# Kernel optimization log

Measured on AMD Instinct MI355X. Metric: run time of the kernel, lower is better.

Reference implementation:

```python
import jax, jax.numpy as jnp
import numpy as np

B, T, C, K = 16, 4096, 64, 1024  # K = codebook rows including pad row 0


def setup_inputs() -> dict:
    key = jax.random.key(0)
    k1, k2, k3 = jax.random.split(key, 3)
    z = jax.random.normal(k1, (B, T, C), dtype=jnp.float32)
    codebook_weight = jax.random.normal(k2, (K, C), dtype=jnp.float32)
    # contiguous valid prefixes of random length (torch loop breaks at first 0)
    lengths = jax.random.randint(k3, (B,), T // 2, T + 1)
    mask = (jnp.arange(T)[None, :] < lengths[:, None]).astype(jnp.float32)[:, :, None]
    return {"z": z, "codebook_weight": codebook_weight, "mask": mask}


def _forward(z, codebook_weight, mask):
    # F.normalize(z, p=2, dim=-1) with eps clamp
    z = z / jnp.clip(jnp.linalg.norm(z, axis=-1, keepdims=True), 1e-12)
    e = jax.lax.stop_gradient(codebook_weight)[1:]  # (K-1, C), detached like torch
    zf = z.reshape(-1, C)                            # (B*T, C)
    # squared euclidean distances: ||z||^2 + ||e||^2 - 2 z e^T
    d = (zf * zf).sum(1, keepdims=True) + (e * e).sum(1)[None, :] - 2.0 * (zf @ e.T)
    idx = jnp.argmin(d, axis=1).reshape(B, T)        # (B, T) codes in [0, K-2]
    # scatter(one-hot) @ e  ==  gather rows of e
    z_q = e[idx] * mask                              # (B, T, C)

    valid_count = mask.sum()
    commitment_loss = (jnp.square(z - jax.lax.stop_gradient(z_q)) * mask).sum() / valid_count

    # straight-through estimator
    z_q = z + z_q - jax.lax.stop_gradient(z)

    m1 = mask[:, 1:, :]
    smoothness_loss = (jnp.square(z_q[:, :-1, :] - z_q[:, 1:, :]) * m1).sum() / m1.sum()

    # --- parallel RLE (replaces the host-side python loop) ---
    # torch loop breaks at first mask==0 -> only contiguous valid prefix matters
    mvalid = jnp.cumprod(mask[..., 0], axis=1) > 0   # (B, T) bool
    change = idx[:, 1:] != idx[:, :-1]
    # position 0 always starts a segment; new segment where code changes inside valid prefix
    is_start = jnp.concatenate(
        [jnp.ones((B, 1), dtype=bool), change & mvalid[:, 1:]], axis=1)  # (B, T)
    # stable argsort puts start positions first, in increasing time order
    order = jnp.argsort(jnp.where(is_start, 0, 1), axis=1)               # (B, T)
    n = is_start.sum(axis=1)                                             # segments per batch
    sel_mask = jnp.arange(T)[None, :] < n[:, None]                        # (B, T)
    sel_pos = jnp.where(sel_mask, order, 0)                               # padded to T
    n_mask = sel_mask.astype(jnp.float32)[..., None]                      # (B, T, 1)
    n_z_q = jnp.take_along_axis(z_q, sel_pos[:, :, None], axis=1) * n_mask
    selected_encodings = jnp.where(
        sel_mask, jnp.take_along_axis(idx, sel_pos, axis=1) + 1, 0)       # (B, T) int
    return smoothness_loss, commitment_loss, z_q, n_z_q, n_mask, selected_encodings


def reference(z, codebook_weight, mask):
    return _forward(z, codebook_weight, mask)
```

## Files before the change

### kernel.cpp

```cpp
#include <hip/hip_runtime.h>
#include <math.h>

typedef __attribute__((ext_vector_type(8))) short short8;
typedef __attribute__((ext_vector_type(4))) float f32x4;

#define B_  16
#define T_  4096
#define C_  64
#define KE_ 1023
#define BT_ (B_ * T_)
#define WINHALF 5e-4f


__device__ __forceinline__ unsigned short f2bf(float x) {
    unsigned int u = __float_as_uint(x);
    unsigned int r = (u + 0x7FFFu + ((u >> 16) & 1u)) >> 16;
    return (unsigned short)r;
}
__device__ __forceinline__ float bf2f(unsigned short h) {
    return __uint_as_float(((unsigned int)h) << 16);
}

typedef __attribute__((address_space(1))) const unsigned int g_u32;
typedef __attribute__((address_space(3))) unsigned int l_u32;
__device__ __forceinline__ void gload16(const void* g, void* l) {
    __builtin_amdgcn_global_load_lds((g_u32*)g, (l_u32*)l, 16, 0, 0);
}

__global__ __launch_bounds__(256) void k_prep(const float* __restrict__ cb,
                                              float* __restrict__ ee,
                                              float* __restrict__ ee2,
                                              unsigned short* __restrict__ Eh,
                                              unsigned short* __restrict__ El,
                                              int* __restrict__ flagcnt) {
    const int k = blockIdx.x * 256 + threadIdx.x;
    if (k == 0) *flagcnt = 0;
    unsigned int* EhU = (unsigned int*)Eh;
    unsigned int* ElU = (unsigned int*)El;
    if (k < KE_) {
        const float* r = cb + (size_t)(k + 1) * C_;
        float s = 0.f;
        #pragma unroll
        for (int c = 0; c < C_; c += 2) {
            const float x0 = r[c], x1 = r[c + 1];
            s = fmaf(x0, x0, s);
            s = fmaf(x1, x1, s);
            const float n0 = -x0, n1 = -x1;
            const unsigned short h0 = f2bf(n0), h1 = f2bf(n1);
            const unsigned short l0 = f2bf(n0 - bf2f(h0));
            const unsigned short l1 = f2bf(n1 - bf2f(h1));
            EhU[k * 32 + c / 2] = (unsigned int)h0 | ((unsigned int)h1 << 16);
            ElU[k * 32 + c / 2] = (unsigned int)l0 | ((unsigned int)l1 << 16);
        }
        ee[k]  = s;
        ee2[k] = 0.5f + 0.5f * s;
    } else {
        #pragma unroll
        for (int c = 0; c < 32; ++c) { EhU[k * 32 + c] = 0u; ElU[k * 32 + c] = 0u; }
        ee[k]  = INFINITY;
        ee2[k] = INFINITY;
    }
}

__global__ __launch_bounds__(256, 2) void k_assign(
    const float* __restrict__ z, const unsigned short* __restrict__ Eh,
    const unsigned short* __restrict__ El, const float* __restrict__ ee2,
    int* __restrict__ kbest, int* __restrict__ flaglist,
    int* __restrict__ flagcnt) {

    __shared__ __align__(16) unsigned short s_eh[2][128 * 64];
    __shared__ __align__(16) unsigned short s_el[2][128 * 64];
    __shared__ float s_ee[2][128];

    const int tid  = threadIdx.x;
    const int wave = tid >> 6;
    const int lane = tid & 63;
    const int col  = lane & 15;
    const int quad = lane >> 4;
    const int Q0   = blockIdx.x * 128 + wave * 32;

    short8 ah[2][2], al[2][2];
    #pragma unroll
    for (int g = 0; g < 2; ++g) {
        const float4* zp = (const float4*)(z + (size_t)(Q0 + g * 16 + col) * C_);
        const float4 f0 = zp[quad * 2];
        const float4 f1 = zp[quad * 2 + 1];
        const float4 f2 = zp[8 + quad * 2];
        const float4 f3 = zp[8 + quad * 2 + 1];
        float xs[16] = {f0.x, f0.y, f0.z, f0.w, f1.x, f1.y, f1.z, f1.w,
                        f2.x, f2.y, f2.z, f2.w, f3.x, f3.y, f3.z, f3.w};
        float ss = 0.f;
        #pragma unroll
        for (int i = 0; i < 16; ++i) ss = fmaf(xs[i], xs[i], ss);
        ss += __shfl_xor(ss, 16);
        ss += __shfl_xor(ss, 32);
        const float inv = 1.f / fmaxf(sqrtf(ss), 1e-12f);
        short8 h0, h1, l0, l1;
        #pragma unroll
        for (int i = 0; i < 8; ++i) {
            const float x = xs[i] * inv;
            const unsigned short hx = f2bf(x);
            h0[i] = (short)hx;
            l0[i] = (short)f2bf(x - bf2f(hx));
            const float y = xs[8 + i] * inv;
            const unsigned short hy = f2bf(y);
            h1[i] = (short)hy;
            l1[i] = (short)f2bf(y - bf2f(hy));
        }
        ah[g][0] = h0; ah[g][1] = h1;
        al[g][0] = l0; al[g][1] = l1;
    }

    float bestv[2][4], secv[2][4];
    int   bkk[2][4];
    #pragma unroll
    for (int g = 0; g < 2; ++g)
        #pragma unroll
        for (int r = 0; r < 4; ++r) {
            bestv[g][r] = INFINITY; secv[g][r] = INFINITY; bkk[g][r] = 0;
        }

    const int srow = tid >> 3;
    const int schk = (tid & 7) ^ (srow & 7);
    const int ldsb = (wave * 8) * 64;

#define STAGE(tt, bb) do {                                                     \
        _Pragma("unroll")                                                      \
        for (int j = 0; j < 4; ++j) {                                          \
            const size_t go = (size_t)((tt) * 128 + j * 32 + srow) * 64        \
                              + (size_t)schk * 8;                              \
            gload16(Eh + go, (void*)&s_eh[bb][ldsb + j * 32 * 64]);            \
            gload16(El + go, (void*)&s_el[bb][ldsb + j * 32 * 64]);            \
        }                                                                      \
        if (tid < 128) s_ee[bb][tid] = ee2[(tt) * 128 + tid];                  \
    } while (0)

    int cur = 0;
    STAGE(0, 0);
    __syncthreads();

    const int coff = (quad ^ (col & 7)) * 8;

    for (int t = 0; t < 8; ++t) {
        if (t < 7) STAGE(t + 1, cur ^ 1);

        float ev[8];
        #pragma unroll
        for (int s = 0; s < 8; ++s) ev[s] = s_ee[cur][s * 16 + col];

        #pragma unroll 2
        for (int s = 0; s < 8; ++s) {
            const int rb = (s * 16 + col) * 64;
            const short8 bh0 = *(const short8*)&s_eh[cur][rb + coff];
            const short8 bh1 = *(const short8*)&s_eh[cur][rb + (coff ^ 32)];
            const short8 bl0 = *(const short8*)&s_el[cur][rb + coff];
            const short8 bl1 = *(const short8*)&s_el[cur][rb + (coff ^ 32)];

            const float e2 = ev[s];
            f32x4 p0 = {e2, e2, e2, e2}, p1 = {e2, e2, e2, e2};
            f32x4 q0 = {0.f, 0.f, 0.f, 0.f}, q1 = {0.f, 0.f, 0.f, 0.f};
            p0 = __builtin_amdgcn_mfma_f32_16x16x32_bf16(ah[0][0], bh0, p0, 0, 0, 0);
            p1 = __builtin_amdgcn_mfma_f32_16x16x32_bf16(ah[1][0], bh0, p1, 0, 0, 0);
            q0 = __builtin_amdgcn_mfma_f32_16x16x32_bf16(ah[0][1], bh1, q0, 0, 0, 0);
            q1 = __builtin_amdgcn_mfma_f32_16x16x32_bf16(ah[1][1], bh1, q1, 0, 0, 0);
            p0 = __builtin_amdgcn_mfma_f32_16x16x32_bf16(ah[0][0], bl0, p0, 0, 0, 0);
            p1 = __builtin_amdgcn_mfma_f32_16x16x32_bf16(ah[1][0], bl0, p1, 0, 0, 0);
            q0 = __builtin_amdgcn_mfma_f32_16x16x32_bf16(ah[0][1], bl1, q0, 0, 0, 0);
            q1 = __builtin_amdgcn_mfma_f32_16x16x32_bf16(ah[1][1], bl1, q1, 0, 0, 0);
            p0 = __builtin_amdgcn_mfma_f32_16x16x32_bf16(al[0][0], bh0, p0, 0, 0, 0);
            p1 = __builtin_amdgcn_mfma_f32_16x16x32_bf16(al[1][0], bh0, p1, 0, 0, 0);
            q0 = __builtin_amdgcn_mfma_f32_16x16x32_bf16(al[0][1], bh1, q0, 0, 0, 0);
            q1 = __builtin_amdgcn_mfma_f32_16x16x32_bf16(al[1][1], bh1, q1, 0, 0, 0);

            const int kc = t * 128 + s * 16 + col;
            #pragma unroll
            for (int r = 0; r < 4; ++r) {
                {
                    const float v = p0[r] + q0[r];
                    const bool lt = v < bestv[0][r];
                    secv[0][r]  = lt ? bestv[0][r] : fminf(secv[0][r], v);
                    bkk[0][r]   = lt ? kc : bkk[0][r];
                    bestv[0][r] = lt ? v : bestv[0][r];
                }
                {
                    const float v = p1[r] + q1[r];
                    const bool lt = v < bestv[1][r];
                    secv[1][r]  = lt ? bestv[1][r] : fminf(secv[1][r], v);
                    bkk[1][r]   = lt ? kc : bkk[1][r];
                    bestv[1][r] = lt ? v : bestv[1][r];
                }
            }
        }
        __syncthreads();
        cur ^= 1;
    }
#undef STAGE

    #pragma unroll
    for (int g = 0; g < 2; ++g) {
        #pragma unroll
        for (int r = 0; r < 4; ++r) {
            float b  = bestv[g][r], sc = secv[g][r];
            int   k  = bkk[g][r];
            #pragma unroll
            for (int off = 1; off < 16; off <<= 1) {
                const float ob = __shfl_xor(b, off);
                const int   ok = __shfl_xor(k, off);
                const float os = __shfl_xor(sc, off);
                const bool take = (ob < b) || (ob == b && ok < k);
                const float lose = take ? b : ob;
                sc = fminf(fminf(sc, os), lose);
                b  = take ? ob : b;
                k  = take ? ok : k;
            }
            if (col == 0) {
                const int q = Q0 + g * 16 + quad * 4 + r;
                kbest[q] = k;
                if (!(sc - b > WINHALF)) {
                    const int pos = atomicAdd(flagcnt, 1);
                    flaglist[pos] = q;
                }
            }
        }
    }
}

__global__ __launch_bounds__(256) void k_fix(const float* __restrict__ z,
                                             const float* __restrict__ cb,
                                             const float* __restrict__ ee,
                                             const int* __restrict__ flagcnt,
                                             const int* __restrict__ flaglist,
                                             int* __restrict__ kbest) {
    __shared__ float s_z[64];
    __shared__ float s_bv[4];
    __shared__ int   s_bk[4];
    const int tid  = threadIdx.x;
    const int lane = tid & 63;
    const int wave = tid >> 6;
    const int n = *flagcnt;

    for (int i = blockIdx.x; i < n; i += 1024) {
        const int q = flaglist[i];
        __syncthreads();
        if (tid < 16) ((float4*)s_z)[tid] = ((const float4*)(z + (size_t)q * C_))[tid];
        __syncthreads();

        float4 zn[16];
        float ss = 0.f;
        #pragma unroll
        for (int c4 = 0; c4 < 16; ++c4) {
            const float4 v = ((const float4*)s_z)[c4];
            zn[c4] = v;
            ss = fmaf(v.x, v.x, ss); ss = fmaf(v.y, v.y, ss);
            ss = fmaf(v.z, v.z, ss); ss = fmaf(v.w, v.w, ss);
        }
        const float nrm = fmaxf(sqrtf(ss), 1e-12f);
        #pragma unroll
        for (int c4 = 0; c4 < 16; ++c4) {
            zn[c4].x /= nrm; zn[c4].y /= nrm; zn[c4].z /= nrm; zn[c4].w /= nrm;
        }

        const int k0 = tid * 4;
        const float4* e0 = (const float4*)(cb + (size_t)(k0 + 1) * C_);
        const float4* e1 = (const float4*)(cb + (size_t)(k0 + 2) * C_);
        const float4* e2 = (const float4*)(cb + (size_t)(k0 + 3) * C_);
        const float4* e3 = (const float4*)(cb + (size_t)((k0 + 4 <= KE_) ? (k0 + 4) : KE_) * C_);
        float d0 = 0.f, d1 = 0.f, d2 = 0.f, d3 = 0.f;
        #pragma unroll
        for (int c4 = 0; c4 < 16; ++c4) {
            const float4 x = zn[c4];
            const float4 a = e0[c4], b = e1[c4], c = e2[c4], d = e3[c4];
            d0 = fmaf(x.x, a.x, d0); d0 = fmaf(x.y, a.y, d0);
            d0 = fmaf(x.z, a.z, d0); d0 = fmaf(x.w, a.w, d0);
            d1 = fmaf(x.x, b.x, d1); d1 = fmaf(x.y, b.y, d1);
            d1 = fmaf(x.z, b.z, d1); d1 = fmaf(x.w, b.w, d1);
            d2 = fmaf(x.x, c.x, d2); d2 = fmaf(x.y, c.y, d2);
            d2 = fmaf(x.z, c.z, d2); d2 = fmaf(x.w, c.w, d2);
            d3 = fmaf(x.x, d.x, d3); d3 = fmaf(x.y, d.y, d3);
            d3 = fmaf(x.z, d.z, d3); d3 = fmaf(x.w, d.w, d3);
        }
        float bv = INFINITY;
        int   bk = 0;
        float v;
        v = fmaf(-2.f, d0, ee[k0 + 0]); if (v < bv) { bv = v; bk = k0 + 0; }
        v = fmaf(-2.f, d1, ee[k0 + 1]); if (v < bv) { bv = v; bk = k0 + 1; }
        v = fmaf(-2.f, d2, ee[k0 + 2]); if (v < bv) { bv = v; bk = k0 + 2; }
        v = fmaf(-2.f, d3, ee[k0 + 3]); if (v < bv) { bv = v; bk = k0 + 3; }

        #pragma unroll
        for (int off = 32; off > 0; off >>= 1) {
            const float ov = __shfl_down(bv, off);
            const int   ok = __shfl_down(bk, off);
            if (ov < bv || (ov == bv && ok < bk)) { bv = ov; bk = ok; }
        }
        if (lane == 0) { s_bv[wave] = bv; s_bk[wave] = bk; }
        __syncthreads();
        if (tid == 0) {
            float fb = s_bv[0]; int fk = s_bk[0];
            #pragma unroll
            for (int w = 1; w < 4; ++w) {
                if (s_bv[w] < fb || (s_bv[w] == fb && s_bk[w] < fk)) {
                    fb = s_bv[w]; fk = s_bk[w];
                }
            }
            kbest[q] = fk;
        }
    }
}

__global__ __launch_bounds__(256) void k_epi(
    const float* __restrict__ z, const float* __restrict__ cb,
    const float* __restrict__ mask, const int* __restrict__ kbest,
    float* __restrict__ zqo,
    float* __restrict__ commit_part, float* __restrict__ valid_part,
    float* __restrict__ smooth_part) {

    __shared__ float s_red[12];
    const int tid  = threadIdx.x;
    const int lane = tid & 63;
    const int wave = tid >> 6;
    const int q    = blockIdx.x * 256 + tid;

    const int bi = kbest[q];
    const float m     = mask[q];
    const float mnext = (lane != 63) ? mask[q + 1] : 0.f;

    const float4* zp = (const float4*)(z + (size_t)q * C_);
    const float4* er = (const float4*)(cb + (size_t)(bi + 1) * C_);
    float4* zo = (float4*)(zqo + (size_t)q * C_);

    float4 zr[16];
    float ss = 0.f;
    #pragma unroll
    for (int i = 0; i < 16; ++i) {
        float4 v = zp[i];
        zr[i] = v;
        ss = fmaf(v.x, v.x, ss); ss = fmaf(v.y, v.y, ss);
        ss = fmaf(v.z, v.z, ss); ss = fmaf(v.w, v.w, ss);
    }
    const float nrm = fmaxf(sqrtf(ss), 1e-12f);

    float commit = 0.f, sm = 0.f;
    #pragma unroll
    for (int c4 = 0; c4 < 16; ++c4) {
        const float z0 = zr[c4].x / nrm, z1 = zr[c4].y / nrm;
        const float z2 = zr[c4].z / nrm, z3 = zr[c4].w / nrm;
        const float4 e4 = er[c4];
        const float q0 = e4.x * m, q1 = e4.y * m, q2 = e4.z * m, q3 = e4.w * m;
        float4 o;
        o.x = (z0 + q0) - z0;
        o.y = (z1 + q1) - z1;
        o.z = (z2 + q2) - z2;
        o.w = (z3 + q3) - z3;
        zo[c4] = o;
        const float d0 = z0 - q0, d1 = z1 - q1, d2 = z2 - q2, d3 = z3 - q3;
        commit = fmaf(d0, d0, commit); commit = fmaf(d1, d1, commit);
        commit = fmaf(d2, d2, commit); commit = fmaf(d3, d3, commit);
        const float n0 = __shfl_down(o.x, 1);
        const float n1 = __shfl_down(o.y, 1);
        const float n2 = __shfl_down(o.z, 1);
        const float n3 = __shfl_down(o.w, 1);
        const float x0 = o.x - n0, x1 = o.y - n1;
        const float x2 = o.z - n2, x3 = o.w - n3;
        sm = fmaf(x0, x0, sm); sm = fmaf(x1, x1, sm);
        sm = fmaf(x2, x2, sm); sm = fmaf(x3, x3, sm);
    }
    commit *= m;
    sm     *= mnext;
    float vc = m;
    #pragma unroll
    for (int off = 32; off > 0; off >>= 1) {
        commit += __shfl_down(commit, off);
        vc     += __shfl_down(vc, off);
        sm     += __shfl_down(sm, off);
    }
    if (lane == 0) { s_red[wave] = commit; s_red[4 + wave] = vc; s_red[8 + wave] = sm; }
    __syncthreads();
    if (tid == 0) {
        commit_part[blockIdx.x] = s_red[0] + s_red[1] + s_red[2] + s_red[3];
        valid_part[blockIdx.x]  = s_red[4] + s_red[5] + s_red[6] + s_red[7];
        smooth_part[blockIdx.x] = s_red[8] + s_red[9] + s_red[10] + s_red[11];
    }
}

__global__ __launch_bounds__(256) void k_scan(const int* __restrict__ kbest,
                                              const float* __restrict__ mask,
                                              const float* __restrict__ zqo,
                                              int* __restrict__ selpos,
                                              int* __restrict__ nst,
                                              float* __restrict__ smooth_part) {
    __shared__ int cnt[256];
    __shared__ float sred[4];
    const int b = blockIdx.x;
    const int tid = threadIdx.x;
    const int base = b * T_;
    const int t0 = tid * 16;

    int flags = 0, c = 0;
    int prev = (tid == 0) ? -1 : kbest[base + t0 - 1];
    #pragma unroll
    for (int i = 0; i < 16; ++i) {
        const int t = t0 + i;
        const int cur = kbest[base + t];
        const int is = (t == 0) ? 1
                     : ((cur != prev && mask[base + t] > 0.f) ? 1 : 0);
        flags |= is << i;
        c += is;
        prev = cur;
    }
    cnt[tid] = c;
    __syncthreads();
    for (int off = 1; off < 256; off <<= 1) {
        int add = (tid >= off) ? cnt[tid - off] : 0;
        __syncthreads();
        cnt[tid] += add;
        __syncthreads();
    }
    int pos = cnt[tid] - c;
    #pragma unroll
    for (int i = 0; i < 16; ++i) {
        if ((flags >> i) & 1) selpos[base + pos++] = t0 + i;
    }
    if (tid == 255) nst[b] = cnt[255];

    float v = 0.f;
    for (int e = tid; e < 63 * 64; e += 256) {
        const int j = e >> 6, cc = e & 63;
        const int t = j * 64 + 63;
        const int qq = base + t;
        const float d = zqo[(size_t)qq * C_ + cc] - zqo[(size_t)(qq + 1) * C_ + cc];
        v = fmaf(d * mask[qq + 1], d, v);
    }
    #pragma unroll
    for (int off = 32; off > 0; off >>= 1) v += __shfl_down(v, off);
    if ((tid & 63) == 0) sred[tid >> 6] = v;
    __syncthreads();
    if (tid == 0) smooth_part[256 + b] = sred[0] + sred[1] + sred[2] + sred[3];
}

__global__ __launch_bounds__(256) void k_gsel(const float* __restrict__ zqo,
                                              const int* __restrict__ kbest,
                                              const int* __restrict__ selpos,
                                              const int* __restrict__ nst,
                                              const float* __restrict__ commit_part,
                                              const float* __restrict__ valid_part,
                                              const float* __restrict__ smooth_part,
                                              float* __restrict__ nzq,
                                              float* __restrict__ nmask,
                                              float* __restrict__ sel,
                                              float* __restrict__ out) {
    const int gid = blockIdx.x * 256 + threadIdx.x;
    const int b   = gid >> 16;
    const int rem = gid & 65535;
    const int j   = rem >> 4;
    const int c4  = rem & 15;
    const int n   = nst[b];
    float4 v = make_float4(0.f, 0.f, 0.f, 0.f);
    int p = 0;
    if (j < n) {
        p = selpos[b * T_ + j];
        v = ((const float4*)zqo)[((size_t)b * T_ + p) * 16 + c4];
    }
    ((float4*)nzq)[gid] = v;
    if (c4 == 0) {
        float nm = 0.f, s = 0.f;
        if (j < n) { nm = 1.f; s = (float)(kbest[b * T_ + p] + 1); }
        nmask[b * T_ + j] = nm;
        sel[b * T_ + j]   = s;
    }

    if (blockIdx.x == 0) {
        __shared__ double rc[256];
        __shared__ double rv[256];
        __shared__ double rs[256];
        const int tid = threadIdx.x;
        double sc = (double)commit_part[tid];
        double sv = (double)valid_part[tid];
        double ssm = (double)smooth_part[tid];
        if (tid < 16) ssm += (double)smooth_part[256 + tid];
        rc[tid] = sc; rv[tid] = sv; rs[tid] = ssm;
        __syncthreads();
        for (int off = 128; off > 0; off >>= 1) {
            if (tid < off) {
                rc[tid] += rc[tid + off];
                rv[tid] += rv[tid + off];
                rs[tid] += rs[tid + off];
            }
            __syncthreads();
        }
        if (tid == 0) {
            double valid = rv[0];
            out[0] = (float)(rs[0] / (valid - (double)B_));
            out[1] = (float)(rc[0] / valid);
        }
    }
}

extern "C" void kernel_launch(void* const* d_in, const int* in_sizes, int n_in,
                              void* d_out, int out_size, void* d_ws, size_t ws_size,
                              hipStream_t stream) {
    const float* z    = (const float*)d_in[0];
    const float* cb   = (const float*)d_in[1];
    const float* mask = (const float*)d_in[2];
    float* out = (float*)d_out;
    char* ws = (char*)d_ws;

    int*            flagcnt     = (int*)(ws + 0);
    float*          ee          = (float*)(ws + 64);
    unsigned short* Eh          = (unsigned short*)(ws + 4224);
    unsigned short* El          = (unsigned short*)(ws + 135296);
    int*            kbest       = (int*)(ws + 266368);
    int*            selpos      = (int*)(ws + 528512);
    int*            nst         = (int*)(ws + 790656);
    float*          commit_part = (float*)(ws + 791680);
    float*          valid_part  = (float*)(ws + 792704);
    float*          smooth_part = (float*)(ws + 793728);
    int*            flaglist    = (int*)(ws + 794816);
    float*          ee2         = (float*)(ws + 1056960);

    float* zqo   = out + 2;
    float* nzq   = zqo + (size_t)BT_ * C_;
    float* nmask = nzq + (size_t)BT_ * C_;
    float* sel   = nmask + BT_;

    k_prep  <<<4,    256, 0, stream>>>(cb, ee, ee2, Eh, El, flagcnt);
    k_assign<<<512,  256, 0, stream>>>(z, Eh, El, ee2, kbest, flaglist, flagcnt);
    k_fix   <<<1024, 256, 0, stream>>>(z, cb, ee, flagcnt, flaglist, kbest);
    k_epi   <<<256,  256, 0, stream>>>(z, cb, mask, kbest, zqo,
                                       commit_part, valid_part, smooth_part);
    k_scan  <<<B_,   256, 0, stream>>>(kbest, mask, zqo, selpos, nst, smooth_part);
    k_gsel  <<<4096, 256, 0, stream>>>(zqo, kbest, selpos, nst,
                                       commit_part, valid_part, smooth_part,
                                       nzq, nmask, sel, out);
}
```

Baseline: 160.0 us.

## Split k_assign work across 8 waves with one 16-row query group each

```diff
diff --git a/kernel.cpp b/kernel.cpp
--- a/kernel.cpp
+++ b/kernel.cpp
@@ -62,7 +62,7 @@
     }
 }
 
-__global__ __launch_bounds__(256, 2) void k_assign(
+__global__ __launch_bounds__(512, 4) void k_assign(
     const float* __restrict__ z, const unsigned short* __restrict__ Eh,
     const unsigned short* __restrict__ El, const float* __restrict__ ee2,
     int* __restrict__ kbest, int* __restrict__ flaglist,
@@ -77,12 +77,11 @@
     const int lane = tid & 63;
     const int col  = lane & 15;
     const int quad = lane >> 4;
-    const int Q0   = blockIdx.x * 128 + wave * 32;
-
-    short8 ah[2][2], al[2][2];
-    #pragma unroll
-    for (int g = 0; g < 2; ++g) {
-        const float4* zp = (const float4*)(z + (size_t)(Q0 + g * 16 + col) * C_);
+    const int Q0   = blockIdx.x * 128 + wave * 16;
+
+    short8 ah[2], al[2];
+    {
+        const float4* zp = (const float4*)(z + (size_t)(Q0 + col) * C_);
         const float4 f0 = zp[quad * 2];
         const float4 f1 = zp[quad * 2 + 1];
         const float4 f2 = zp[8 + quad * 2];
@@ -107,30 +106,28 @@
             h1[i] = (short)hy;
             l1[i] = (short)f2bf(y - bf2f(hy));
         }
-        ah[g][0] = h0; ah[g][1] = h1;
-        al[g][0] = l0; al[g][1] = l1;
-    }
-
-    float bestv[2][4], secv[2][4];
-    int   bkk[2][4];
-    #pragma unroll
-    for (int g = 0; g < 2; ++g)
-        #pragma unroll
-        for (int r = 0; r < 4; ++r) {
-            bestv[g][r] = INFINITY; secv[g][r] = INFINITY; bkk[g][r] = 0;
-        }
+        ah[0] = h0; ah[1] = h1;
+        al[0] = l0; al[1] = l1;
+    }
+
+    float bestv[4], secv[4];
+    int   bkk[4];
+    #pragma unroll
+    for (int r = 0; r < 4; ++r) {
+        bestv[r] = INFINITY; secv[r] = INFINITY; bkk[r] = 0;
+    }
 
     const int srow = tid >> 3;
     const int schk = (tid & 7) ^ (srow & 7);
-    const int ldsb = (wave * 8) * 64;
+    const int ldsb = wave * 512;
 
 #define STAGE(tt, bb) do {                                                     \
         _Pragma("unroll")                                                      \
-        for (int j = 0; j < 4; ++j) {                                          \
-            const size_t go = (size_t)((tt) * 128 + j * 32 + srow) * 64        \
+        for (int j = 0; j < 2; ++j) {                                          \
+            const size_t go = (size_t)((tt) * 128 + j * 64 + srow) * 64        \
                               + (size_t)schk * 8;                              \
-            gload16(Eh + go, (void*)&s_eh[bb][ldsb + j * 32 * 64]);            \
-            gload16(El + go, (void*)&s_el[bb][ldsb + j * 32 * 64]);            \
+            gload16(Eh + go, (void*)&s_eh[bb][j * 4096 + ldsb]);               \
+            gload16(El + go, (void*)&s_el[bb][j * 4096 + ldsb]);               \
         }                                                                      \
         if (tid < 128) s_ee[bb][tid] = ee2[(tt) * 128 + tid];                  \
     } while (0)
@@ -157,38 +154,23 @@
             const short8 bl1 = *(const short8*)&s_el[cur][rb + (coff ^ 32)];
 
             const float e2 = ev[s];
-            f32x4 p0 = {e2, e2, e2, e2}, p1 = {e2, e2, e2, e2};
-            f32x4 q0 = {0.f, 0.f, 0.f, 0.f}, q1 = {0.f, 0.f, 0.f, 0.f};
-            p0 = __builtin_amdgcn_mfma_f32_16x16x32_bf16(ah[0][0], bh0, p0, 0, 0, 0);
-            p1 = __builtin_amdgcn_mfma_f32_16x16x32_bf16(ah[1][0], bh0, p1, 0, 0, 0);
-            q0 = __builtin_amdgcn_mfma_f32_16x16x32_bf16(ah[0][1], bh1, q0, 0, 0, 0);
-            q1 = __builtin_amdgcn_mfma_f32_16x16x32_bf16(ah[1][1], bh1, q1, 0, 0, 0);
-            p0 = __builtin_amdgcn_mfma_f32_16x16x32_bf16(ah[0][0], bl0, p0, 0, 0, 0);
-            p1 = __builtin_amdgcn_mfma_f32_16x16x32_bf16(ah[1][0], bl0, p1, 0, 0, 0);
-            q0 = __builtin_amdgcn_mfma_f32_16x16x32_bf16(ah[0][1], bl1, q0, 0, 0, 0);
-            q1 = __builtin_amdgcn_mfma_f32_16x16x32_bf16(ah[1][1], bl1, q1, 0, 0, 0);
-            p0 = __builtin_amdgcn_mfma_f32_16x16x32_bf16(al[0][0], bh0, p0, 0, 0, 0);
-            p1 = __builtin_amdgcn_mfma_f32_16x16x32_bf16(al[1][0], bh0, p1, 0, 0, 0);
-            q0 = __builtin_amdgcn_mfma_f32_16x16x32_bf16(al[0][1], bh1, q0, 0, 0, 0);
-            q1 = __builtin_amdgcn_mfma_f32_16x16x32_bf16(al[1][1], bh1, q1, 0, 0, 0);
+            f32x4 p0 = {e2, e2, e2, e2};
+            f32x4 q0 = {0.f, 0.f, 0.f, 0.f};
+            p0 = __builtin_amdgcn_mfma_f32_16x16x32_bf16(ah[0], bh0, p0, 0, 0, 0);
+            q0 = __builtin_amdgcn_mfma_f32_16x16x32_bf16(ah[1], bh1, q0, 0, 0, 0);
+            p0 = __builtin_amdgcn_mfma_f32_16x16x32_bf16(ah[0], bl0, p0, 0, 0, 0);
+            q0 = __builtin_amdgcn_mfma_f32_16x16x32_bf16(ah[1], bl1, q0, 0, 0, 0);
+            p0 = __builtin_amdgcn_mfma_f32_16x16x32_bf16(al[0], bh0, p0, 0, 0, 0);
+            q0 = __builtin_amdgcn_mfma_f32_16x16x32_bf16(al[1], bh1, q0, 0, 0, 0);
 
             const int kc = t * 128 + s * 16 + col;
             #pragma unroll
             for (int r = 0; r < 4; ++r) {
-                {
-                    const float v = p0[r] + q0[r];
-                    const bool lt = v < bestv[0][r];
-                    secv[0][r]  = lt ? bestv[0][r] : fminf(secv[0][r], v);
-                    bkk[0][r]   = lt ? kc : bkk[0][r];
-                    bestv[0][r] = lt ? v : bestv[0][r];
-                }
-                {
-                    const float v = p1[r] + q1[r];
-                    const bool lt = v < bestv[1][r];
-                    secv[1][r]  = lt ? bestv[1][r] : fminf(secv[1][r], v);
-                    bkk[1][r]   = lt ? kc : bkk[1][r];
-                    bestv[1][r] = lt ? v : bestv[1][r];
-                }
+                const float v = p0[r] + q0[r];
+                const bool lt = v < bestv[r];
+                secv[r]  = lt ? bestv[r] : fminf(secv[r], v);
+                bkk[r]   = lt ? kc : bkk[r];
+                bestv[r] = lt ? v : bestv[r];
             }
         }
         __syncthreads();
@@ -197,29 +179,26 @@
 #undef STAGE
 
     #pragma unroll
-    for (int g = 0; g < 2; ++g) {
-        #pragma unroll
-        for (int r = 0; r < 4; ++r) {
-            float b  = bestv[g][r], sc = secv[g][r];
-            int   k  = bkk[g][r];
-            #pragma unroll
-            for (int off = 1; off < 16; off <<= 1) {
-                const float ob = __shfl_xor(b, off);
-                const int   ok = __shfl_xor(k, off);
-                const float os = __shfl_xor(sc, off);
-                const bool take = (ob < b) || (ob == b && ok < k);
-                const float lose = take ? b : ob;
-                sc = fminf(fminf(sc, os), lose);
-                b  = take ? ob : b;
-                k  = take ? ok : k;
-            }
-            if (col == 0) {
-                const int q = Q0 + g * 16 + quad * 4 + r;
-                kbest[q] = k;
-                if (!(sc - b > WINHALF)) {
-                    const int pos = atomicAdd(flagcnt, 1);
-                    flaglist[pos] = q;
-                }
+    for (int r = 0; r < 4; ++r) {
+        float b  = bestv[r], sc = secv[r];
+        int   k  = bkk[r];
+        #pragma unroll
+        for (int off = 1; off < 16; off <<= 1) {
+            const float ob = __shfl_xor(b, off);
+            const int   ok = __shfl_xor(k, off);
+            const float os = __shfl_xor(sc, off);
+            const bool take = (ob < b) || (ob == b && ok < k);
+            const float lose = take ? b : ob;
+            sc = fminf(fminf(sc, os), lose);
+            b  = take ? ob : b;
+            k  = take ? ok : k;
+        }
+        if (col == 0) {
+            const int q = Q0 + quad * 4 + r;
+            kbest[q] = k;
+            if (!(sc - b > WINHALF)) {
+                const int pos = atomicAdd(flagcnt, 1);
+                flaglist[pos] = q;
             }
         }
     }
@@ -524,7 +503,7 @@
     float* sel   = nmask + BT_;
 
     k_prep  <<<4,    256, 0, stream>>>(cb, ee, ee2, Eh, El, flagcnt);
-    k_assign<<<512,  256, 0, stream>>>(z, Eh, El, ee2, kbest, flaglist, flagcnt);
+    k_assign<<<512,  512, 0, stream>>>(z, Eh, El, ee2, kbest, flaglist, flagcnt);
     k_fix   <<<1024, 256, 0, stream>>>(z, cb, ee, flagcnt, flaglist, kbest);
     k_epi   <<<256,  256, 0, stream>>>(z, cb, mask, kbest, zqo,
                                        commit_part, valid_part, smooth_part);
```

New measurement: 158.3 us. About the same (-1.1%).

## Software-pipeline LDS fragment loads, split staging, and set MFMA priority

Applied to the files above, without the earlier changes.

```diff
diff --git a/kernel.cpp b/kernel.cpp
--- a/kernel.cpp
+++ b/kernel.cpp
@@ -124,77 +124,91 @@
     const int schk = (tid & 7) ^ (srow & 7);
     const int ldsb = (wave * 8) * 64;
 
-#define STAGE(tt, bb) do {                                                     \
-        _Pragma("unroll")                                                      \
-        for (int j = 0; j < 4; ++j) {                                          \
-            const size_t go = (size_t)((tt) * 128 + j * 32 + srow) * 64        \
-                              + (size_t)schk * 8;                              \
-            gload16(Eh + go, (void*)&s_eh[bb][ldsb + j * 32 * 64]);            \
-            gload16(El + go, (void*)&s_el[bb][ldsb + j * 32 * 64]);            \
-        }                                                                      \
-        if (tid < 128) s_ee[bb][tid] = ee2[(tt) * 128 + tid];                  \
+#define STAGE_J(tt, bb, j) do {                                                \
+        const size_t go = (size_t)((tt) * 128 + (j) * 32 + srow) * 64          \
+                          + (size_t)schk * 8;                                  \
+        gload16(Eh + go, (void*)&s_eh[bb][ldsb + (j) * 2048]);                 \
+        gload16(El + go, (void*)&s_el[bb][ldsb + (j) * 2048]);                 \
     } while (0)
 
     int cur = 0;
-    STAGE(0, 0);
+    #pragma unroll
+    for (int j = 0; j < 4; ++j) STAGE_J(0, 0, j);
+    if (tid < 128) s_ee[0][tid] = ee2[tid];
     __syncthreads();
 
     const int coff = (quad ^ (col & 7)) * 8;
 
     for (int t = 0; t < 8; ++t) {
-        if (t < 7) STAGE(t + 1, cur ^ 1);
+        if (t < 7) { STAGE_J(t + 1, cur ^ 1, 0); STAGE_J(t + 1, cur ^ 1, 1); }
 
         float ev[8];
         #pragma unroll
         for (int s = 0; s < 8; ++s) ev[s] = s_ee[cur][s * 16 + col];
 
-        #pragma unroll 2
+        short8 fh0 = *(const short8*)&s_eh[cur][col * 64 + coff];
+        short8 fh1 = *(const short8*)&s_eh[cur][col * 64 + (coff ^ 32)];
+        short8 fl0 = *(const short8*)&s_el[cur][col * 64 + coff];
+        short8 fl1 = *(const short8*)&s_el[cur][col * 64 + (coff ^ 32)];
+
+        if (t < 7) {
+            STAGE_J(t + 1, cur ^ 1, 2); STAGE_J(t + 1, cur ^ 1, 3);
+            if (tid < 128) s_ee[cur ^ 1][tid] = ee2[(t + 1) * 128 + tid];
+        }
+
+        const int kb = t * 128 + col;
+
+        #pragma unroll
         for (int s = 0; s < 8; ++s) {
-            const int rb = (s * 16 + col) * 64;
-            const short8 bh0 = *(const short8*)&s_eh[cur][rb + coff];
-            const short8 bh1 = *(const short8*)&s_eh[cur][rb + (coff ^ 32)];
-            const short8 bl0 = *(const short8*)&s_el[cur][rb + coff];
-            const short8 bl1 = *(const short8*)&s_el[cur][rb + (coff ^ 32)];
+            const int sn = (s < 7) ? (s + 1) : 7;
+            const int rb = (sn * 16 + col) * 64;
+            short8 nh0 = *(const short8*)&s_eh[cur][rb + coff];
+            short8 nh1 = *(const short8*)&s_eh[cur][rb + (coff ^ 32)];
+            short8 nl0 = *(const short8*)&s_el[cur][rb + coff];
+            short8 nl1 = *(const short8*)&s_el[cur][rb + (coff ^ 32)];
 
             const float e2 = ev[s];
-            f32x4 p0 = {e2, e2, e2, e2}, p1 = {e2, e2, e2, e2};
-            f32x4 q0 = {0.f, 0.f, 0.f, 0.f}, q1 = {0.f, 0.f, 0.f, 0.f};
-            p0 = __builtin_amdgcn_mfma_f32_16x16x32_bf16(ah[0][0], bh0, p0, 0, 0, 0);
-            p1 = __builtin_amdgcn_mfma_f32_16x16x32_bf16(ah[1][0], bh0, p1, 0, 0, 0);
-            q0 = __builtin_amdgcn_mfma_f32_16x16x32_bf16(ah[0][1], bh1, q0, 0, 0, 0);
-            q1 = __builtin_amdgcn_mfma_f32_16x16x32_bf16(ah[1][1], bh1, q1, 0, 0, 0);
-            p0 = __builtin_amdgcn_mfma_f32_16x16x32_bf16(ah[0][0], bl0, p0, 0, 0, 0);
-            p1 = __builtin_amdgcn_mfma_f32_16x16x32_bf16(ah[1][0], bl0, p1, 0, 0, 0);
-            q0 = __builtin_amdgcn_mfma_f32_16x16x32_bf16(ah[0][1], bl1, q0, 0, 0, 0);
-            q1 = __builtin_amdgcn_mfma_f32_16x16x32_bf16(ah[1][1], bl1, q1, 0, 0, 0);
-            p0 = __builtin_amdgcn_mfma_f32_16x16x32_bf16(al[0][0], bh0, p0, 0, 0, 0);
-            p1 = __builtin_amdgcn_mfma_f32_16x16x32_bf16(al[1][0], bh0, p1, 0, 0, 0);
-            q0 = __builtin_amdgcn_mfma_f32_16x16x32_bf16(al[0][1], bh1, q0, 0, 0, 0);
-            q1 = __builtin_amdgcn_mfma_f32_16x16x32_bf16(al[1][1], bh1, q1, 0, 0, 0);
-
-            const int kc = t * 128 + s * 16 + col;
+            f32x4 p0 = {e2, e2, e2, e2};
+            f32x4 p1 = {e2, e2, e2, e2};
+            __builtin_amdgcn_s_setprio(1);
+            p0 = __builtin_amdgcn_mfma_f32_16x16x32_bf16(ah[0][0], fh0, p0, 0, 0, 0);
+            p1 = __builtin_amdgcn_mfma_f32_16x16x32_bf16(ah[1][0], fh0, p1, 0, 0, 0);
+            p0 = __builtin_amdgcn_mfma_f32_16x16x32_bf16(ah[0][1], fh1, p0, 0, 0, 0);
+            p1 = __builtin_amdgcn_mfma_f32_16x16x32_bf16(ah[1][1], fh1, p1, 0, 0, 0);
+            p0 = __builtin_amdgcn_mfma_f32_16x16x32_bf16(ah[0][0], fl0, p0, 0, 0, 0);
+            p1 = __builtin_amdgcn_mfma_f32_16x16x32_bf16(ah[1][0], fl0, p1, 0, 0, 0);
+            p0 = __builtin_amdgcn_mfma_f32_16x16x32_bf16(ah[0][1], fl1, p0, 0, 0, 0);
+            p1 = __builtin_amdgcn_mfma_f32_16x16x32_bf16(ah[1][1], fl1, p1, 0, 0, 0);
+            p0 = __builtin_amdgcn_mfma_f32_16x16x32_bf16(al[0][0], fh0, p0, 0, 0, 0);
+            p1 = __builtin_amdgcn_mfma_f32_16x16x32_bf16(al[1][0], fh0, p1, 0, 0, 0);
+            p0 = __builtin_amdgcn_mfma_f32_16x16x32_bf16(al[0][1], fh1, p0, 0, 0, 0);
+            p1 = __builtin_amdgcn_mfma_f32_16x16x32_bf16(al[1][1], fh1, p1, 0, 0, 0);
+            __builtin_amdgcn_s_setprio(0);
+
+            const int kc = kb + s * 16;
             #pragma unroll
             for (int r = 0; r < 4; ++r) {
                 {
-                    const float v = p0[r] + q0[r];
-                    const bool lt = v < bestv[0][r];
-                    secv[0][r]  = lt ? bestv[0][r] : fminf(secv[0][r], v);
-                    bkk[0][r]   = lt ? kc : bkk[0][r];
-                    bestv[0][r] = lt ? v : bestv[0][r];
+                    const float v  = p0[r];
+                    const float bo = bestv[0][r];
+                    bkk[0][r]   = (v < bo) ? kc : bkk[0][r];
+                    secv[0][r]  = fminf(secv[0][r], fmaxf(bo, v));
+                    bestv[0][r] = fminf(bo, v);
                 }
                 {
-                    const float v = p1[r] + q1[r];
-                    const bool lt = v < bestv[1][r];
-                    secv[1][r]  = lt ? bestv[1][r] : fminf(secv[1][r], v);
-                    bkk[1][r]   = lt ? kc : bkk[1][r];
-                    bestv[1][r] = lt ? v : bestv[1][r];
+                    const float v  = p1[r];
+                    const float bo = bestv[1][r];
+                    bkk[1][r]   = (v < bo) ? kc : bkk[1][r];
+                    secv[1][r]  = fminf(secv[1][r], fmaxf(bo, v));
+                    bestv[1][r] = fminf(bo, v);
                 }
             }
+            fh0 = nh0; fh1 = nh1; fl0 = nl0; fl1 = nl1;
         }
         __syncthreads();
         cur ^= 1;
     }
-#undef STAGE
+#undef STAGE_J
 
     #pragma unroll
     for (int g = 0; g < 2; ++g) {
```

Result: faster. 154.0 us (-3.7%).
